# Performance work log

Hardware: AMD Instinct MI355X
Metric: run time of the kernel (lower is better)

The kernel has to match this reference:

```python
import jax, jax.numpy as jnp
import numpy as np

N = 100000   # nodes
E = 1600000  # edges
IN, HID, OUT = 128, 256, 47


def setup_inputs() -> dict:
    key = jax.random.key(0)
    ks = jax.random.split(key, 12)

    def lin(k, i, o):
        return (jax.random.normal(k, (i, o), jnp.float32) / np.sqrt(i)).astype(jnp.float32)

    x = jax.random.normal(ks[0], (N, IN), jnp.float32)
    edge_index = jax.random.randint(ks[1], (2, E), 0, N, dtype=jnp.int64)
    return {
        "x": x,
        "edge_index": edge_index,
        "Wl0": lin(ks[2], IN, HID), "bl0": jnp.zeros((HID,), jnp.float32), "Wr0": lin(ks[3], IN, HID),
        "Wl1": lin(ks[4], HID, HID), "bl1": jnp.zeros((HID,), jnp.float32), "Wr1": lin(ks[5], HID, HID),
        "Wl2": lin(ks[6], HID, OUT), "bl2": jnp.zeros((OUT,), jnp.float32), "Wr2": lin(ks[7], HID, OUT),
    }


def _sage_conv(x, src, dst, Wl, bl, Wr):
    # PyG SAGEConv default: mean-aggregate source features into destinations,
    # then out = lin_l(agg) + lin_r(x) (bias only on lin_l).
    ones = jnp.ones((src.shape[0],), x.dtype)
    deg = jax.ops.segment_sum(ones, dst, num_segments=N)            # [N]
    summed = jax.ops.segment_sum(x[src], dst, num_segments=N)      # [N, d]
    agg = summed / jnp.maximum(deg, 1.0)[:, None]
    return agg @ Wl + bl + x @ Wr


def reference(x, edge_index, Wl0, bl0, Wr0, Wl1, bl1, Wr1, Wl2, bl2, Wr2):
    src, dst = edge_index[0], edge_index[1]
    h = _sage_conv(x, src, dst, Wl0, bl0, Wr0)
    h = jax.nn.relu(h)  # dropout is identity in eval mode
    h_out = _sage_conv(h, src, dst, Wl1, bl1, Wr1)  # pre-ReLU hidden returned by module
    h = jax.nn.relu(h_out)
    out = _sage_conv(h, src, dst, Wl2, bl2, Wr2)
    return (out, h_out)
```

## Files before the change

kernel.cpp:

```cpp
#include <hip/hip_runtime.h>
#include <cstdint>
#include <cstddef>

static constexpr int DIN  = 128;
static constexpr int DH   = 256;
static constexpr int DOUT = 47;

typedef __attribute__((ext_vector_type(8))) short bf16x8;
typedef __attribute__((ext_vector_type(4))) float f32x4;
typedef __attribute__((ext_vector_type(2))) float f32x2;

__device__ __forceinline__ short f2bf(float f) {
    unsigned u = __float_as_uint(f);
    unsigned r = (u + 0x7fffu + ((u >> 16) & 1u)) >> 16;
    return (short)r;
}

__device__ __forceinline__ void addpk(unsigned w, float* a) {
    f32x2 lo = __builtin_amdgcn_cvt_pk_f32_fp8(w, false);
    f32x2 hi = __builtin_amdgcn_cvt_pk_f32_fp8(w, true);
    a[0] += lo[0]; a[1] += lo[1]; a[2] += hi[0]; a[3] += hi[1];
}
__device__ __forceinline__ unsigned enc4(float a, float b, float c, float d) {
    unsigned w = __builtin_amdgcn_cvt_pk_fp8_f32(a, b, 0, false);
    w = __builtin_amdgcn_cvt_pk_fp8_f32(c, d, w, true);
    return w;
}
__device__ __forceinline__ unsigned char enc1(float v) {
    return (unsigned char)(__builtin_amdgcn_cvt_pk_fp8_f32(v, v, 0, false) & 0xff);
}
__device__ __forceinline__ unsigned pbf2(float a, float b, float sc) {
    return (unsigned)(unsigned short)f2bf(a * sc) |
           ((unsigned)(unsigned short)f2bf(b * sc) << 16);
}

__global__ void k_detect(const int* __restrict__ e, int* __restrict__ flag, int nprobe) {
    int i = blockIdx.x * blockDim.x + threadIdx.x;
    if (i < nprobe) {
        if (e[2 * i + 1] != 0) atomicOr(flag, 1);
    }
}

__global__ void k_hist(const int* __restrict__ e, const int* __restrict__ flag,
                       int* __restrict__ cnt, int E) {
    int i = blockIdx.x * blockDim.x + threadIdx.x;
    if (i >= E) return;
    int is32 = *flag;
    int d = is32 ? e[E + i] : e[2 * (E + i)];
    atomicAdd(&cnt[d], 1);
}

__global__ void k_fill(const int* __restrict__ e, const int* __restrict__ flag,
                       const int* __restrict__ rowptr, int* __restrict__ cursor,
                       int* __restrict__ colbuf, int E) {
    int i = blockIdx.x * blockDim.x + threadIdx.x;
    if (i >= E) return;
    int is32 = *flag;
    int s = is32 ? e[i] : e[2 * i];
    int d = is32 ? e[E + i] : e[2 * (E + i)];
    int pos = atomicAdd(&cursor[d], 1);
    colbuf[rowptr[d] + pos] = s;
}


__launch_bounds__(256)
__global__ void k_binhist(const int* __restrict__ e, const int* __restrict__ flag,
                          int* __restrict__ bucketCnt, int E, int shift, int nbk) {
    __shared__ int h[1024];
    int t = threadIdx.x;
    for (int i = t; i < nbk; i += 256) h[i] = 0;
    __syncthreads();
    int is32 = *flag;
    int stride = gridDim.x * 256;
    for (int i = blockIdx.x * 256 + t; i < E; i += stride) {
        int d = is32 ? e[E + i] : e[2 * (E + i)];
        atomicAdd(&h[d >> shift], 1);
    }
    __syncthreads();
    for (int i = t; i < nbk; i += 256) {
        int v = h[i];
        if (v) atomicAdd(&bucketCnt[i], v);
    }
}

__global__ void k_bucket_scan(const int* __restrict__ bucketCnt, int* __restrict__ bucketOff,
                              int* __restrict__ bucketCur, int nbk, int E) {
    __shared__ int s[1024];
    int t = threadIdx.x;
    int v = (t < nbk) ? bucketCnt[t] : 0;
    s[t] = v;
    __syncthreads();
    for (int off = 1; off < 1024; off <<= 1) {
        int xv = (t >= off) ? s[t - off] : 0;
        __syncthreads();
        s[t] += xv;
        __syncthreads();
    }
    if (t < nbk) { bucketOff[t] = s[t] - v; bucketCur[t] = 0; }
    if (t == 0) bucketOff[nbk] = E;
}

__launch_bounds__(256)
__global__ void k_binscatter(const int* __restrict__ e, const int* __restrict__ flag,
                             const int* __restrict__ bucketOff, int* __restrict__ bucketCur,
                             uint2* __restrict__ pairbuf, int E, int shift, int nbk) {
    __shared__ int h[1024];
    __shared__ int cur[1024];
    int t = threadIdx.x;
    for (int i = t; i < nbk; i += 256) h[i] = 0;
    __syncthreads();
    int is32 = *flag;
    int chunk = (E + gridDim.x - 1) / gridDim.x;
    int lo = blockIdx.x * chunk;
    int hi = lo + chunk < E ? lo + chunk : E;
    for (int i = lo + t; i < hi; i += 256) {
        int d = is32 ? e[E + i] : e[2 * (E + i)];
        atomicAdd(&h[d >> shift], 1);
    }
    __syncthreads();
    for (int i = t; i < nbk; i += 256) {
        int c = h[i];
        int base = c ? atomicAdd(&bucketCur[i], c) : 0;
        h[i] = bucketOff[i] + base;
        cur[i] = 0;
    }
    __syncthreads();
    for (int i = lo + t; i < hi; i += 256) {
        int sv = is32 ? e[i] : e[2 * i];
        int d  = is32 ? e[E + i] : e[2 * (E + i)];
        int b = d >> shift;
        int lp = atomicAdd(&cur[b], 1);
        pairbuf[h[b] + lp] = make_uint2((unsigned)sv, (unsigned)d);
    }
}

__launch_bounds__(256)
__global__ void k_bhist(const uint2* __restrict__ pairbuf, const int* __restrict__ bucketOff,
                        int* __restrict__ cnt, int shift, int N) {
    __shared__ int h[2048];
    int b = blockIdx.x;
    int t = threadIdx.x;
    int first = b << shift;
    int span = (1 << shift);
    if (first + span > N) span = N - first;
    for (int i = t; i < span; i += 256) h[i] = 0;
    __syncthreads();
    int lo = bucketOff[b], hi = bucketOff[b + 1];
    for (int j = lo + t; j < hi; j += 256) {
        int d = (int)pairbuf[j].y;
        atomicAdd(&h[d - first], 1);
    }
    __syncthreads();
    for (int i = t; i < span; i += 256) cnt[first + i] = h[i];
}

#define FILL_CAP 12288
__launch_bounds__(256)
__global__ void k_fill2(const uint2* __restrict__ pairbuf, const int* __restrict__ bucketOff,
                        const int* __restrict__ rowptr, int* __restrict__ cursor,
                        int* __restrict__ colbuf, int shift, int N) {
    __shared__ int cur[2048];
    __shared__ int sbuf[FILL_CAP];
    int b = blockIdx.x;
    int t = threadIdx.x;
    int first = b << shift;
    int span = (1 << shift);
    if (first + span > N) span = N - first;
    int lo = bucketOff[b], hi = bucketOff[b + 1];
    int nEdge = hi - lo;
    int base = rowptr[first];
    if (nEdge <= FILL_CAP) {
        for (int i = t; i < span; i += 256) cur[i] = rowptr[first + i] - base;
        __syncthreads();
        for (int j = lo + t; j < hi; j += 256) {
            uint2 p = pairbuf[j];
            int lp = atomicAdd(&cur[(int)p.y - first], 1);
            sbuf[lp] = (int)p.x;
        }
        __syncthreads();
        for (int i = t; i < nEdge; i += 256) colbuf[base + i] = sbuf[i];
    } else {
        for (int j = lo + t; j < hi; j += 256) {
            uint2 p = pairbuf[j];
            int d = (int)p.y;
            int pos = atomicAdd(&cursor[d], 1);
            colbuf[rowptr[d] + pos] = (int)p.x;
        }
    }
}

__global__ void k_chunk_sum(const int* __restrict__ cnt, int* __restrict__ csum, int n) {
    int base = blockIdx.x * 1024;
    int t = threadIdx.x;
    int s = 0;
#pragma unroll
    for (int j = 0; j < 4; j++) {
        int i = base + t * 4 + j;
        if (i < n) s += cnt[i];
    }
    __shared__ int red[256];
    red[t] = s;
    __syncthreads();
    for (int off = 128; off > 0; off >>= 1) {
        if (t < off) red[t] += red[t + off];
        __syncthreads();
    }
    if (t == 0) csum[blockIdx.x] = red[0];
}

__global__ void k_scan_csum(int* __restrict__ csum, int n,
                            int* __restrict__ rowptr, int N, int E) {
    __shared__ int s[128];
    int t = threadIdx.x;
    int v = (t < n) ? csum[t] : 0;
    s[t] = v;
    __syncthreads();
    for (int off = 1; off < 128; off <<= 1) {
        int xv = (t >= off) ? s[t - off] : 0;
        __syncthreads();
        s[t] += xv;
        __syncthreads();
    }
    if (t < n) csum[t] = s[t] - v;
    if (t == 0) rowptr[N] = E;
}

__global__ void k_scan_apply(const int* __restrict__ cnt, const int* __restrict__ csum,
                             int* __restrict__ rowptr, int n) {
    int base = blockIdx.x * 1024, t = threadIdx.x;
    int i0 = base + t * 4;
    int v[4];
#pragma unroll
    for (int j = 0; j < 4; j++) {
        int i = i0 + j;
        v[j] = (i < n) ? cnt[i] : 0;
    }
    int tsum = v[0] + v[1] + v[2] + v[3];
    __shared__ int s[256];
    s[t] = tsum;
    __syncthreads();
    for (int off = 1; off < 256; off <<= 1) {
        int xv = (t >= off) ? s[t - off] : 0;
        __syncthreads();
        s[t] += xv;
        __syncthreads();
    }
    int excl = s[t] - tsum + csum[blockIdx.x];
#pragma unroll
    for (int j = 0; j < 4; j++) {
        int i = i0 + j;
        if (i < n) rowptr[i] = excl;
        excl += v[j];
    }
}

__global__ void k_invdeg(const int* __restrict__ rowptr, float* __restrict__ invd, int N) {
    int i = blockIdx.x * blockDim.x + threadIdx.x;
    if (i >= N) return;
    int d = rowptr[i + 1] - rowptr[i];
    invd[i] = 1.0f / (float)(d > 1 ? d : 1);
}

__global__ void k_f2bf8(const float* __restrict__ X, short* __restrict__ Yb,
                        unsigned* __restrict__ Y8, int n4) {
    int i = blockIdx.x * 256 + threadIdx.x;
    if (i >= n4) return;
    float4 v = *(const float4*)(X + (size_t)i * 4);
    short4 o;
    o.x = f2bf(v.x); o.y = f2bf(v.y); o.z = f2bf(v.z); o.w = f2bf(v.w);
    *(short4*)(Yb + (size_t)i * 4) = o;
    Y8[i] = enc4(v.x, v.y, v.z, v.w);
}

__global__ void k_pack(const float* __restrict__ W, short* __restrict__ P,
                       int ksteps, int Nt, int Ncols) {
    int idx = blockIdx.x * 256 + threadIdx.x;
    int total = ksteps * Nt * 64;
    if (idx >= total) return;
    int lane = idx & 63;
    int t = idx >> 6;
    int nt = t % Nt;
    int ks = t / Nt;
    int n = nt * 16 + (lane & 15);
    int kb = ks * 32 + (lane >> 4) * 8;
    bf16x8 o;
#pragma unroll
    for (int j = 0; j < 8; j++)
        o[j] = (n < Ncols) ? f2bf(W[(size_t)(kb + j) * Ncols + n]) : (short)0;
    *(bf16x8*)(P + (size_t)idx * 8) = o;
}

__launch_bounds__(256)
__global__ void k_agg256_f8(const unsigned char* __restrict__ X8, const int* __restrict__ rowptr,
                            const int* __restrict__ colv, const float* __restrict__ invd,
                            short* __restrict__ out, int N) {
    const int lane = threadIdx.x & 63;
    const int node = blockIdx.x * 4 + (threadIdx.x >> 6);
    if (node >= N) return;
    int beg = __builtin_amdgcn_readfirstlane(rowptr[node]);
    int end = __builtin_amdgcn_readfirstlane(rowptr[node + 1]);
    const int q = lane >> 4, sub = lane & 15;
    const unsigned char* Xs = X8 + sub * 16;

    float acc[16];
#pragma unroll
    for (int c = 0; c < 16; c++) acc[c] = 0.f;

    auto addv = [&](uint4 a) {
        addpk(a.x, acc); addpk(a.y, acc + 4); addpk(a.z, acc + 8); addpk(a.w, acc + 12);
    };

    int j = beg;
    for (; j + 7 < end; j += 8) {
        int i0 = colv[j], i1 = colv[j + 1], i2 = colv[j + 2], i3 = colv[j + 3];
        int i4 = colv[j + 4], i5 = colv[j + 5], i6 = colv[j + 6], i7 = colv[j + 7];
        int sA = (q == 0) ? i0 : (q == 1) ? i1 : (q == 2) ? i2 : i3;
        int sB = (q == 0) ? i4 : (q == 1) ? i5 : (q == 2) ? i6 : i7;
        uint4 a = *(const uint4*)(Xs + (size_t)sA * 256);
        uint4 b = *(const uint4*)(Xs + (size_t)sB * 256);
        addv(a); addv(b);
    }
    if (j + 3 < end) {
        int i0 = colv[j], i1 = colv[j + 1], i2 = colv[j + 2], i3 = colv[j + 3];
        int sA = (q == 0) ? i0 : (q == 1) ? i1 : (q == 2) ? i2 : i3;
        uint4 a = *(const uint4*)(Xs + (size_t)sA * 256);
        addv(a);
        j += 4;
    }
    int rem = end - j;
    if (rem > 0) {
        int i0 = colv[j];
        int i1 = rem > 1 ? colv[j + 1] : i0;
        int i2 = rem > 2 ? colv[j + 2] : i0;
        int s = (q == 1) ? i1 : (q == 2) ? i2 : i0;
        uint4 a = *(const uint4*)(Xs + (size_t)s * 256);
        if (q < rem) addv(a);
    }

#pragma unroll
    for (int c = 0; c < 16; c++) {
        acc[c] += __shfl_xor(acc[c], 16);
        acc[c] += __shfl_xor(acc[c], 32);
    }

    if (q == 0) {
        float sc = invd[node];
        uint4 o0, o1;
        o0.x = pbf2(acc[0], acc[1], sc);   o0.y = pbf2(acc[2], acc[3], sc);
        o0.z = pbf2(acc[4], acc[5], sc);   o0.w = pbf2(acc[6], acc[7], sc);
        o1.x = pbf2(acc[8], acc[9], sc);   o1.y = pbf2(acc[10], acc[11], sc);
        o1.z = pbf2(acc[12], acc[13], sc); o1.w = pbf2(acc[14], acc[15], sc);
        short* op = out + (size_t)node * 256 + sub * 16;
        *(uint4*)op = o0;
        *(uint4*)(op + 8) = o1;
    }
}

__launch_bounds__(256)
__global__ void k_agg128_f8(const unsigned char* __restrict__ X8, const int* __restrict__ rowptr,
                            const int* __restrict__ colv, const float* __restrict__ invd,
                            short* __restrict__ out, int N) {
    const int lane = threadIdx.x & 63;
    const int node = blockIdx.x * 4 + (threadIdx.x >> 6);
    if (node >= N) return;
    int beg = __builtin_amdgcn_readfirstlane(rowptr[node]);
    int end = __builtin_amdgcn_readfirstlane(rowptr[node + 1]);
    const int grp = lane >> 3, sub = lane & 7;
    const unsigned char* Xs = X8 + sub * 16;

    float acc[16];
#pragma unroll
    for (int c = 0; c < 16; c++) acc[c] = 0.f;

    auto addv = [&](uint4 a) {
        addpk(a.x, acc); addpk(a.y, acc + 4); addpk(a.z, acc + 8); addpk(a.w, acc + 12);
    };

    int j = beg;
    for (; j + 15 < end; j += 16) {
        int sA = colv[j + grp];
        int sB = colv[j + 8 + grp];
        uint4 a = *(const uint4*)(Xs + (size_t)sA * 128);
        uint4 b = *(const uint4*)(Xs + (size_t)sB * 128);
        addv(a); addv(b);
    }
    if (j + 7 < end) {
        int sA = colv[j + grp];
        uint4 a = *(const uint4*)(Xs + (size_t)sA * 128);
        addv(a);
        j += 8;
    }
    int rem = end - j;
    if (rem > 0) {
        int sA = colv[j + (grp < rem ? grp : 0)];
        uint4 a = *(const uint4*)(Xs + (size_t)sA * 128);
        if (grp < rem) addv(a);
    }

#pragma unroll
    for (int c = 0; c < 16; c++) {
        acc[c] += __shfl_xor(acc[c], 8);
        acc[c] += __shfl_xor(acc[c], 16);
        acc[c] += __shfl_xor(acc[c], 32);
    }

    if (grp == 0) {
        float sc = invd[node];
        uint4 o0, o1;
        o0.x = pbf2(acc[0], acc[1], sc);   o0.y = pbf2(acc[2], acc[3], sc);
        o0.z = pbf2(acc[4], acc[5], sc);   o0.w = pbf2(acc[6], acc[7], sc);
        o1.x = pbf2(acc[8], acc[9], sc);   o1.y = pbf2(acc[10], acc[11], sc);
        o1.z = pbf2(acc[12], acc[13], sc); o1.w = pbf2(acc[14], acc[15], sc);
        short* op = out + (size_t)node * 128 + sub * 16;
        *(uint4*)op = o0;
        *(uint4*)(op + 8) = o1;
    }
}

__launch_bounds__(256, 4)
__global__ void k_gemm_mfma_wide(const short* __restrict__ A1, const short* A2,
                                 const short* __restrict__ P1, const short* __restrict__ P2,
                                 const float* __restrict__ bias,
                                 float* Cf, short* Cb, unsigned char* C8,
                                 int M, int K1, int K2) {
    const int lane = threadIdx.x & 63;
    const int wave = threadIdx.x >> 6;
    const int quad = lane >> 4;
    const int r    = lane & 15;
    const int rowBase = blockIdx.x * 32;

    f32x4 acc[2][4];
#pragma unroll
    for (int mt = 0; mt < 2; mt++)
#pragma unroll
        for (int nt = 0; nt < 4; nt++) acc[mt][nt] = (f32x4)(0.f);

    int arow[2];
#pragma unroll
    for (int mt = 0; mt < 2; mt++) {
        int row = rowBase + mt * 16 + r;
        arow[mt] = row < M ? row : M - 1;
    }

    for (int src = 0; src < 2; src++) {
        const short* A = src ? A2 : A1;
        const short* P = src ? P2 : P1;
        const int K = src ? K2 : K1;
        const int nks = K >> 5;

        bf16x8 af[2], bfr[4];
#pragma unroll
        for (int mt = 0; mt < 2; mt++)
            af[mt] = *(const bf16x8*)(A + (size_t)arow[mt] * K + quad * 8);
#pragma unroll
        for (int nt = 0; nt < 4; nt++)
            bfr[nt] = *(const bf16x8*)(P + (((size_t)(wave * 4 + nt) * 64 + lane) << 3));

        for (int ks = 0; ks < nks; ks++) {
            const int ksn = (ks + 1 < nks) ? ks + 1 : ks;
            bf16x8 afn[2], bfn[4];
#pragma unroll
            for (int mt = 0; mt < 2; mt++)
                afn[mt] = *(const bf16x8*)(A + (size_t)arow[mt] * K + ksn * 32 + quad * 8);
#pragma unroll
            for (int nt = 0; nt < 4; nt++)
                bfn[nt] = *(const bf16x8*)(P + (((size_t)(ksn * 16 + wave * 4 + nt) * 64 + lane) << 3));
#pragma unroll
            for (int mt = 0; mt < 2; mt++)
#pragma unroll
                for (int nt = 0; nt < 4; nt++)
                    acc[mt][nt] = __builtin_amdgcn_mfma_f32_16x16x32_bf16(
                        af[mt], bfr[nt], acc[mt][nt], 0, 0, 0);
#pragma unroll
            for (int mt = 0; mt < 2; mt++) af[mt] = afn[mt];
#pragma unroll
            for (int nt = 0; nt < 4; nt++) bfr[nt] = bfn[nt];
        }
    }

    __syncthreads();

    float bv[4];
#pragma unroll
    for (int nt = 0; nt < 4; nt++) bv[nt] = bias[wave * 64 + nt * 16 + r];

#pragma unroll
    for (int mt = 0; mt < 2; mt++) {
#pragma unroll
        for (int reg = 0; reg < 4; reg++) {
            int row = rowBase + mt * 16 + quad * 4 + reg;
            if (row >= M) continue;
#pragma unroll
            for (int nt = 0; nt < 4; nt++) {
                int col = wave * 64 + nt * 16 + r;
                float v = acc[mt][nt][reg] + bv[nt];
                if (Cf) Cf[(size_t)row * 256 + col] = v;
                if (Cb) Cb[(size_t)row * 256 + col] = f2bf(fmaxf(v, 0.f));
                if (C8) C8[(size_t)row * 256 + col] = enc1(fmaxf(v, 0.f));
            }
        }
    }
}

__launch_bounds__(256, 4)
__global__ void k_gemm_mfma_out(const short* __restrict__ A,
                                const short* __restrict__ Pl, const short* __restrict__ Pr,
                                const float* __restrict__ bias,
                                unsigned char* __restrict__ U8, float* __restrict__ Out, int M) {
    const int lane = threadIdx.x & 63;
    const int wave = threadIdx.x >> 6;
    const int quad = lane >> 4;
    const int r    = lane & 15;
    const int rowBase = blockIdx.x * 128 + wave * 32;

    f32x4 aU[2][3], aO[2][3];
#pragma unroll
    for (int mt = 0; mt < 2; mt++)
#pragma unroll
        for (int nt = 0; nt < 3; nt++) { aU[mt][nt] = (f32x4)(0.f); aO[mt][nt] = (f32x4)(0.f); }

    int arow[2];
#pragma unroll
    for (int mt = 0; mt < 2; mt++) {
        int row = rowBase + mt * 16 + r;
        arow[mt] = row < M ? row : M - 1;
    }

    bf16x8 af[2];
#pragma unroll
    for (int mt = 0; mt < 2; mt++)
        af[mt] = *(const bf16x8*)(A + (size_t)arow[mt] * 256 + quad * 8);

    for (int ks = 0; ks < 8; ks++) {
        const int ksn = (ks + 1 < 8) ? ks + 1 : ks;
        bf16x8 afn[2], bl[3], br[3];
#pragma unroll
        for (int mt = 0; mt < 2; mt++)
            afn[mt] = *(const bf16x8*)(A + (size_t)arow[mt] * 256 + ksn * 32 + quad * 8);
#pragma unroll
        for (int nt = 0; nt < 3; nt++) {
            size_t fo = (((size_t)(ks * 3 + nt) * 64 + lane) << 3);
            bl[nt] = *(const bf16x8*)(Pl + fo);
            br[nt] = *(const bf16x8*)(Pr + fo);
        }
#pragma unroll
        for (int mt = 0; mt < 2; mt++)
#pragma unroll
            for (int nt = 0; nt < 3; nt++) {
                aU[mt][nt] = __builtin_amdgcn_mfma_f32_16x16x32_bf16(af[mt], bl[nt], aU[mt][nt], 0, 0, 0);
                aO[mt][nt] = __builtin_amdgcn_mfma_f32_16x16x32_bf16(af[mt], br[nt], aO[mt][nt], 0, 0, 0);
            }
#pragma unroll
        for (int mt = 0; mt < 2; mt++) af[mt] = afn[mt];
    }

    float bv[3];
#pragma unroll
    for (int nt = 0; nt < 3; nt++) {
        int col = nt * 16 + r;
        bv[nt] = (col < DOUT) ? bias[col] : 0.f;
    }

#pragma unroll
    for (int mt = 0; mt < 2; mt++) {
#pragma unroll
        for (int reg = 0; reg < 4; reg++) {
            int row = rowBase + mt * 16 + quad * 4 + reg;
            if (row >= M) continue;
#pragma unroll
            for (int nt = 0; nt < 3; nt++) {
                int col = nt * 16 + r;
                U8[(size_t)row * 48 + col] = enc1(aU[mt][nt][reg]);
                if (col < DOUT) Out[(size_t)row * DOUT + col] = aO[mt][nt][reg] + bv[nt];
            }
        }
    }
}

__launch_bounds__(256)
__global__ void k_agg_add47_f8(const unsigned char* __restrict__ U8, const int* __restrict__ rowptr,
                               const int* __restrict__ colv, const float* __restrict__ invd,
                               float* __restrict__ out0, int N) {
    const int lane = threadIdx.x & 63;
    const int node = blockIdx.x * 4 + (threadIdx.x >> 6);
    if (node >= N) return;
    int beg = __builtin_amdgcn_readfirstlane(rowptr[node]);
    int end = __builtin_amdgcn_readfirstlane(rowptr[node + 1]);
    const int q = lane >> 4, sub = lane & 15;
    const bool act = sub < 12;
    const unsigned char* Us = U8 + sub * 4;

    float acc[4] = {0.f, 0.f, 0.f, 0.f};

    int j = beg;
    for (; j + 7 < end; j += 8) {
        int i0 = colv[j], i1 = colv[j + 1], i2 = colv[j + 2], i3 = colv[j + 3];
        int i4 = colv[j + 4], i5 = colv[j + 5], i6 = colv[j + 6], i7 = colv[j + 7];
        int sA = (q == 0) ? i0 : (q == 1) ? i1 : (q == 2) ? i2 : i3;
        int sB = (q == 0) ? i4 : (q == 1) ? i5 : (q == 2) ? i6 : i7;
        if (act) {
            unsigned a = *(const unsigned*)(Us + (size_t)sA * 48);
            unsigned b = *(const unsigned*)(Us + (size_t)sB * 48);
            addpk(a, acc); addpk(b, acc);
        }
    }
    if (j + 3 < end) {
        int i0 = colv[j], i1 = colv[j + 1], i2 = colv[j + 2], i3 = colv[j + 3];
        int sA = (q == 0) ? i0 : (q == 1) ? i1 : (q == 2) ? i2 : i3;
        if (act) {
            unsigned a = *(const unsigned*)(Us + (size_t)sA * 48);
            addpk(a, acc);
        }
        j += 4;
    }
    int rem = end - j;
    if (rem > 0) {
        int i0 = colv[j];
        int i1 = rem > 1 ? colv[j + 1] : i0;
        int i2 = rem > 2 ? colv[j + 2] : i0;
        int s = (q == 1) ? i1 : (q == 2) ? i2 : i0;
        if (act && q < rem) {
            unsigned a = *(const unsigned*)(Us + (size_t)s * 48);
            addpk(a, acc);
        }
    }

#pragma unroll
    for (int c = 0; c < 4; c++) {
        acc[c] += __shfl_xor(acc[c], 16);
        acc[c] += __shfl_xor(acc[c], 32);
    }

    if (q == 0 && act) {
        float sc = invd[node];
        int f0 = sub * 4;
        float* op = out0 + (size_t)node * DOUT;
#pragma unroll
        for (int c = 0; c < 4; c++)
            if (f0 + c < DOUT) op[f0 + c] += sc * acc[c];
    }
}

extern "C" void kernel_launch(void* const* d_in, const int* in_sizes, int n_in,
                              void* d_out, int out_size, void* d_ws, size_t ws_size,
                              hipStream_t stream) {
    const float* x   = (const float*)d_in[0];
    const int*   ei  = (const int*)d_in[1];
    const float* Wl0 = (const float*)d_in[2];
    const float* bl0 = (const float*)d_in[3];
    const float* Wr0 = (const float*)d_in[4];
    const float* Wl1 = (const float*)d_in[5];
    const float* bl1 = (const float*)d_in[6];
    const float* Wr1 = (const float*)d_in[7];
    const float* Wl2 = (const float*)d_in[8];
    const float* bl2 = (const float*)d_in[9];
    const float* Wr2 = (const float*)d_in[10];

    const int N = in_sizes[0] / DIN;
    const int E = in_sizes[1] / 2;

    char* p = (char*)d_ws;
    auto alloc = [&](size_t bytes) -> char* {
        char* r = p;
        p += (bytes + 255) & ~(size_t)255;
        return r;
    };
    int*   flag   = (int*)alloc(4);
    int*   cnt    = (int*)alloc((size_t)N * 4);
    int*   rowptr = (int*)alloc((size_t)(N + 1) * 4);
    int*   csum   = (int*)alloc(1024 * 4);
    int*   colbuf = (int*)alloc((size_t)E * 4 + 64);
    float* invd   = (float*)alloc((size_t)N * 4);
    int*   bucketCnt = (int*)alloc(1025 * 4);
    int*   bucketOff = (int*)alloc(1025 * 4);
    int*   bucketCur = (int*)alloc(1024 * 4);
    short* xbf    = (short*)alloc((size_t)N * DIN * 2);
    short* bufA   = (short*)alloc((size_t)N * DH * 2);
    short* h0     = (short*)alloc((size_t)N * DH * 2);
    unsigned*      x8 = (unsigned*)alloc((size_t)N * DIN);
    unsigned char* h8 = (unsigned char*)alloc((size_t)N * DH);
    short* Pl0    = (short*)alloc((size_t)DIN * 256 * 2);
    short* Pr0    = (short*)alloc((size_t)DIN * 256 * 2);
    short* Pl1    = (short*)alloc((size_t)DH * 256 * 2);
    short* Pr1    = (short*)alloc((size_t)DH * 256 * 2);
    short* Pl2    = (short*)alloc((size_t)DH * 48 * 2);
    short* Pr2    = (short*)alloc((size_t)DH * 48 * 2);

    float* out0 = (float*)d_out;
    float* hout = (float*)d_out + (size_t)N * DOUT;

    int span_shift = 7;
    while ((((N - 1) >> span_shift) + 1) > 1024 && span_shift < 21) span_shift++;
    const int NBK = ((N - 1) >> span_shift) + 1;
    const bool fast_csr = (NBK <= 1024) && ((1 << span_shift) <= 2048) &&
                          ((size_t)E * 8 <= (size_t)N * DH * 2);
    uint2* pairbuf = (uint2*)bufA;

    hipMemsetAsync(flag, 0, 4, stream);
    hipMemsetAsync(cnt, 0, (size_t)N * 4, stream);
    hipMemsetAsync(bucketCnt, 0, (size_t)NBK * 4, stream);

    const int nprobe = E < 4096 ? E : 4096;
    k_detect<<<(nprobe + 255) / 256, 256, 0, stream>>>(ei, flag, nprobe);
    if (fast_csr) {
        k_binhist<<<256, 256, 0, stream>>>(ei, flag, bucketCnt, E, span_shift, NBK);
        k_bucket_scan<<<1, 1024, 0, stream>>>(bucketCnt, bucketOff, bucketCur, NBK, E);
        k_binscatter<<<256, 256, 0, stream>>>(ei, flag, bucketOff, bucketCur, pairbuf, E, span_shift, NBK);
        k_bhist<<<NBK, 256, 0, stream>>>(pairbuf, bucketOff, cnt, span_shift, N);
    } else {
        k_hist<<<(E + 255) / 256, 256, 0, stream>>>(ei, flag, cnt, E);
    }
    const int nchunks = (N + 1023) / 1024;
    k_chunk_sum<<<nchunks, 256, 0, stream>>>(cnt, csum, N);
    k_scan_csum<<<1, 128, 0, stream>>>(csum, nchunks, rowptr, N, E);
    k_scan_apply<<<nchunks, 256, 0, stream>>>(cnt, csum, rowptr, N);
    hipMemsetAsync(cnt, 0, (size_t)N * 4, stream);
    if (fast_csr) {
        k_fill2<<<NBK, 256, 0, stream>>>(pairbuf, bucketOff, rowptr, cnt, colbuf, span_shift, N);
    } else {
        k_fill<<<(E + 255) / 256, 256, 0, stream>>>(ei, flag, rowptr, cnt, colbuf, E);
    }
    k_invdeg<<<(N + 255) / 256, 256, 0, stream>>>(rowptr, invd, N);

    k_pack<<<(4 * 16 * 64 + 255) / 256, 256, 0, stream>>>(Wl0, Pl0, 4, 16, 256);
    k_pack<<<(4 * 16 * 64 + 255) / 256, 256, 0, stream>>>(Wr0, Pr0, 4, 16, 256);
    k_pack<<<(8 * 16 * 64 + 255) / 256, 256, 0, stream>>>(Wl1, Pl1, 8, 16, 256);
    k_pack<<<(8 * 16 * 64 + 255) / 256, 256, 0, stream>>>(Wr1, Pr1, 8, 16, 256);
    k_pack<<<(8 * 3 * 64 + 255) / 256, 256, 0, stream>>>(Wl2, Pl2, 8, 3, DOUT);
    k_pack<<<(8 * 3 * 64 + 255) / 256, 256, 0, stream>>>(Wr2, Pr2, 8, 3, DOUT);
    k_f2bf8<<<((N * DIN / 4) + 255) / 256, 256, 0, stream>>>(x, xbf, x8, N * DIN / 4);

    const int aggBlocks = (N + 3) / 4;
    const int gw = (N + 31) / 32;

    k_agg128_f8<<<aggBlocks, 256, 0, stream>>>((const unsigned char*)x8, rowptr, colbuf, invd, bufA, N);
    k_gemm_mfma_wide<<<gw, 256, 0, stream>>>(bufA, xbf, Pl0, Pr0, bl0,
                                             nullptr, h0, h8, N, DIN, DIN);

    k_agg256_f8<<<aggBlocks, 256, 0, stream>>>(h8, rowptr, colbuf, invd, bufA, N);
    k_gemm_mfma_wide<<<gw, 256, 0, stream>>>(bufA, h0, Pl1, Pr1, bl1,
                                             hout, h0, nullptr, N, DH, DH);

    unsigned char* U8 = (unsigned char*)xbf;
    k_gemm_mfma_out<<<(N + 127) / 128, 256, 0, stream>>>(h0, Pl2, Pr2, bl2, U8, out0, N);
    k_agg_add47_f8<<<aggBlocks, 256, 0, stream>>>(U8, rowptr, colbuf, invd, out0, N);
}
```

Before: 631.6 us.

## Store GEMM A operands in MFMA fragment-tiled bf16 layout

The bf16 activation buffers (xbf, aggregated features, h0) are now written in a tile-major layout that matches the per-lane MFMA A-fragment order, so the GEMM kernels read each fragment as one contiguous 16-byte-per-lane coalesced load instead of strided row reads. The aggregation, conversion, and GEMM epilogue writers are changed to emit this layout, and buffers are padded to a multiple of 16 rows so the old row clamping can be removed. In exchange, the epilogue's bf16 stores become scattered 2-byte writes, and all producers and consumers must agree on the new indexing.

```diff
diff --git a/kernel.cpp b/kernel.cpp
--- a/kernel.cpp
+++ b/kernel.cpp
@@ -33,6 +33,7 @@
     return (unsigned)(unsigned short)f2bf(a * sc) |
            ((unsigned)(unsigned short)f2bf(b * sc) << 16);
 }
+
 
 __global__ void k_detect(const int* __restrict__ e, int* __restrict__ flag, int nprobe) {
     int i = blockIdx.x * blockDim.x + threadIdx.x;
@@ -61,7 +62,6 @@
     int pos = atomicAdd(&cursor[d], 1);
     colbuf[rowptr[d] + pos] = s;
 }
-
 
 __launch_bounds__(256)
 __global__ void k_binhist(const int* __restrict__ e, const int* __restrict__ flag,
@@ -262,14 +262,30 @@
 }
 
 __global__ void k_f2bf8(const float* __restrict__ X, short* __restrict__ Yb,
-                        unsigned* __restrict__ Y8, int n4) {
-    int i = blockIdx.x * 256 + threadIdx.x;
-    if (i >= n4) return;
-    float4 v = *(const float4*)(X + (size_t)i * 4);
-    short4 o;
-    o.x = f2bf(v.x); o.y = f2bf(v.y); o.z = f2bf(v.z); o.w = f2bf(v.w);
-    *(short4*)(Yb + (size_t)i * 4) = o;
-    Y8[i] = enc4(v.x, v.y, v.z, v.w);
+                        unsigned* __restrict__ Y8, int nTiles, int N) {
+    int t = blockIdx.x * 256 + threadIdx.x;
+    int total = nTiles * 4 * 64;
+    if (t >= total) return;
+    int lane = t & 63;
+    int kt = t >> 6;
+    int ks = kt & 3;
+    int tile = kt >> 2;
+    int q = (lane >> 4) & 3;
+    int r = lane & 15;
+    int row = tile * 16 + r;
+    int col = ks * 32 + q * 8;
+    bf16x8 o = (bf16x8)(short)0;
+    if (row < N) {
+        const float* src = X + (size_t)row * DIN + col;
+        float4 v0 = *(const float4*)src;
+        float4 v1 = *(const float4*)(src + 4);
+        o[0] = f2bf(v0.x); o[1] = f2bf(v0.y); o[2] = f2bf(v0.z); o[3] = f2bf(v0.w);
+        o[4] = f2bf(v1.x); o[5] = f2bf(v1.y); o[6] = f2bf(v1.z); o[7] = f2bf(v1.w);
+        unsigned* p8 = Y8 + ((size_t)row * DIN + col) / 4;
+        p8[0] = enc4(v0.x, v0.y, v0.z, v0.w);
+        p8[1] = enc4(v1.x, v1.y, v1.z, v1.w);
+    }
+    *(bf16x8*)(Yb + (size_t)t * 8) = o;
 }
 
 __global__ void k_pack(const float* __restrict__ W, short* __restrict__ P,
@@ -350,9 +366,11 @@
         o0.z = pbf2(acc[4], acc[5], sc);   o0.w = pbf2(acc[6], acc[7], sc);
         o1.x = pbf2(acc[8], acc[9], sc);   o1.y = pbf2(acc[10], acc[11], sc);
         o1.z = pbf2(acc[12], acc[13], sc); o1.w = pbf2(acc[14], acc[15], sc);
-        short* op = out + (size_t)node * 256 + sub * 16;
-        *(uint4*)op = o0;
-        *(uint4*)(op + 8) = o1;
+        const int tile = node >> 4, r = node & 15;
+        const int ksC = sub >> 1, q1 = (sub & 1) * 2;
+        size_t base = ((size_t)(tile * 8 + ksC) * 64 + r) * 8;
+        *(uint4*)(out + base + (size_t)q1 * 128)       = o0;
+        *(uint4*)(out + base + (size_t)(q1 + 1) * 128) = o1;
     }
 }
 
@@ -411,9 +429,11 @@
         o0.z = pbf2(acc[4], acc[5], sc);   o0.w = pbf2(acc[6], acc[7], sc);
         o1.x = pbf2(acc[8], acc[9], sc);   o1.y = pbf2(acc[10], acc[11], sc);
         o1.z = pbf2(acc[12], acc[13], sc); o1.w = pbf2(acc[14], acc[15], sc);
-        short* op = out + (size_t)node * 128 + sub * 16;
-        *(uint4*)op = o0;
-        *(uint4*)(op + 8) = o1;
+        const int tile = node >> 4, r = node & 15;
+        const int ksC = sub >> 1, q1 = (sub & 1) * 2;
+        size_t base = ((size_t)(tile * 4 + ksC) * 64 + r) * 8;
+        *(uint4*)(out + base + (size_t)q1 * 128)       = o0;
+        *(uint4*)(out + base + (size_t)(q1 + 1) * 128) = o1;
     }
 }
 
@@ -428,19 +448,13 @@
     const int quad = lane >> 4;
     const int r    = lane & 15;
     const int rowBase = blockIdx.x * 32;
+    const int tile0 = blockIdx.x * 2;
 
     f32x4 acc[2][4];
 #pragma unroll
     for (int mt = 0; mt < 2; mt++)
 #pragma unroll
         for (int nt = 0; nt < 4; nt++) acc[mt][nt] = (f32x4)(0.f);
-
-    int arow[2];
-#pragma unroll
-    for (int mt = 0; mt < 2; mt++) {
-        int row = rowBase + mt * 16 + r;
-        arow[mt] = row < M ? row : M - 1;
-    }
 
     for (int src = 0; src < 2; src++) {
         const short* A = src ? A2 : A1;
@@ -451,7 +465,7 @@
         bf16x8 af[2], bfr[4];
 #pragma unroll
         for (int mt = 0; mt < 2; mt++)
-            af[mt] = *(const bf16x8*)(A + (size_t)arow[mt] * K + quad * 8);
+            af[mt] = *(const bf16x8*)(A + (((size_t)(tile0 + mt) * nks * 64 + lane) << 3));
 #pragma unroll
         for (int nt = 0; nt < 4; nt++)
             bfr[nt] = *(const bf16x8*)(P + (((size_t)(wave * 4 + nt) * 64 + lane) << 3));
@@ -461,7 +475,7 @@
             bf16x8 afn[2], bfn[4];
 #pragma unroll
             for (int mt = 0; mt < 2; mt++)
-                afn[mt] = *(const bf16x8*)(A + (size_t)arow[mt] * K + ksn * 32 + quad * 8);
+                afn[mt] = *(const bf16x8*)(A + ((((size_t)(tile0 + mt) * nks + ksn) * 64 + lane) << 3));
 #pragma unroll
             for (int nt = 0; nt < 4; nt++)
                 bfn[nt] = *(const bf16x8*)(P + (((size_t)(ksn * 16 + wave * 4 + nt) * 64 + lane) << 3));
@@ -488,14 +502,20 @@
     for (int mt = 0; mt < 2; mt++) {
 #pragma unroll
         for (int reg = 0; reg < 4; reg++) {
-            int row = rowBase + mt * 16 + quad * 4 + reg;
+            int rC = quad * 4 + reg;
+            int row = rowBase + mt * 16 + rC;
             if (row >= M) continue;
 #pragma unroll
             for (int nt = 0; nt < 4; nt++) {
                 int col = wave * 64 + nt * 16 + r;
                 float v = acc[mt][nt][reg] + bv[nt];
                 if (Cf) Cf[(size_t)row * 256 + col] = v;
-                if (Cb) Cb[(size_t)row * 256 + col] = f2bf(fmaxf(v, 0.f));
+                if (Cb) {
+                    int ksC = wave * 2 + (nt >> 1);
+                    int qC  = (nt & 1) * 2 + (r >> 3);
+                    size_t d = ((((size_t)(tile0 + mt) * 8 + ksC) * 64 + qC * 16 + rC) << 3) + (r & 7);
+                    Cb[d] = f2bf(fmaxf(v, 0.f));
+                }
                 if (C8) C8[(size_t)row * 256 + col] = enc1(fmaxf(v, 0.f));
             }
         }
@@ -512,6 +532,7 @@
     const int quad = lane >> 4;
     const int r    = lane & 15;
     const int rowBase = blockIdx.x * 128 + wave * 32;
+    const int tile0 = blockIdx.x * 8 + wave * 2;
 
     f32x4 aU[2][3], aO[2][3];
 #pragma unroll
@@ -519,24 +540,17 @@
 #pragma unroll
         for (int nt = 0; nt < 3; nt++) { aU[mt][nt] = (f32x4)(0.f); aO[mt][nt] = (f32x4)(0.f); }
 
-    int arow[2];
-#pragma unroll
-    for (int mt = 0; mt < 2; mt++) {
-        int row = rowBase + mt * 16 + r;
-        arow[mt] = row < M ? row : M - 1;
-    }
-
     bf16x8 af[2];
 #pragma unroll
     for (int mt = 0; mt < 2; mt++)
-        af[mt] = *(const bf16x8*)(A + (size_t)arow[mt] * 256 + quad * 8);
+        af[mt] = *(const bf16x8*)(A + (((size_t)(tile0 + mt) * 8 * 64 + lane) << 3));
 
     for (int ks = 0; ks < 8; ks++) {
         const int ksn = (ks + 1 < 8) ? ks + 1 : ks;
         bf16x8 afn[2], bl[3], br[3];
 #pragma unroll
         for (int mt = 0; mt < 2; mt++)
-            afn[mt] = *(const bf16x8*)(A + (size_t)arow[mt] * 256 + ksn * 32 + quad * 8);
+            afn[mt] = *(const bf16x8*)(A + ((((size_t)(tile0 + mt) * 8 + ksn) * 64 + lane) << 3));
 #pragma unroll
         for (int nt = 0; nt < 3; nt++) {
             size_t fo = (((size_t)(ks * 3 + nt) * 64 + lane) << 3);
@@ -658,6 +672,8 @@
 
     const int N = in_sizes[0] / DIN;
     const int E = in_sizes[1] / 2;
+    const int nTiles = (N + 15) / 16;
+    const size_t Mpad = (size_t)nTiles * 16 + 32;
 
     char* p = (char*)d_ws;
     auto alloc = [&](size_t bytes) -> char* {
@@ -674,9 +690,9 @@
     int*   bucketCnt = (int*)alloc(1025 * 4);
     int*   bucketOff = (int*)alloc(1025 * 4);
     int*   bucketCur = (int*)alloc(1024 * 4);
-    short* xbf    = (short*)alloc((size_t)N * DIN * 2);
-    short* bufA   = (short*)alloc((size_t)N * DH * 2);
-    short* h0     = (short*)alloc((size_t)N * DH * 2);
+    short* xbf    = (short*)alloc(Mpad * DIN * 2);
+    short* bufA   = (short*)alloc(Mpad * DH * 2);
+    short* h0     = (short*)alloc(Mpad * DH * 2);
     unsigned*      x8 = (unsigned*)alloc((size_t)N * DIN);
     unsigned char* h8 = (unsigned char*)alloc((size_t)N * DH);
     short* Pl0    = (short*)alloc((size_t)DIN * 256 * 2);
@@ -693,7 +709,7 @@
     while ((((N - 1) >> span_shift) + 1) > 1024 && span_shift < 21) span_shift++;
     const int NBK = ((N - 1) >> span_shift) + 1;
     const bool fast_csr = (NBK <= 1024) && ((1 << span_shift) <= 2048) &&
-                          ((size_t)E * 8 <= (size_t)N * DH * 2);
+                          ((size_t)E * 8 <= Mpad * DH * 2);
     uint2* pairbuf = (uint2*)bufA;
 
     hipMemsetAsync(flag, 0, 4, stream);
@@ -728,7 +744,7 @@
     k_pack<<<(8 * 16 * 64 + 255) / 256, 256, 0, stream>>>(Wr1, Pr1, 8, 16, 256);
     k_pack<<<(8 * 3 * 64 + 255) / 256, 256, 0, stream>>>(Wl2, Pl2, 8, 3, DOUT);
     k_pack<<<(8 * 3 * 64 + 255) / 256, 256, 0, stream>>>(Wr2, Pr2, 8, 3, DOUT);
-    k_f2bf8<<<((N * DIN / 4) + 255) / 256, 256, 0, stream>>>(x, xbf, x8, N * DIN / 4);
+    k_f2bf8<<<nTiles, 256, 0, stream>>>(x, xbf, x8, nTiles, N);
 
     const int aggBlocks = (N + 3) / 4;
     const int gw = (N + 31) / 32;
```

After: 610.7 us. 3.3% less time.
